# Kernel tuning notes

Hardware: AMD Instinct MI355X
Metric: run time of the kernel (lower is better)

Reference implementation:

```python
import jax
import jax.numpy as jnp
from jax import lax
import numpy as np

B, C, Hsp, Wsp = 16, 256, 64, 64
E, HID = 4, 128          # num_experts, expert_hidden
RH = 128                 # router_hidden
TOP_K = 1
EPS = 1e-9


def setup_inputs() -> dict:
    key = jax.random.key(0)
    ks = jax.random.split(key, 8)
    s = lambda *shape: 1.0 / np.sqrt(shape[-1])
    x = jax.random.normal(ks[0], (B, C, Hsp, Wsp), dtype=jnp.float32)
    # router: Linear(C->RH), Linear(RH->E)
    Wr1 = jax.random.normal(ks[1], (RH, C), dtype=jnp.float32) * s(RH, C)
    br1 = jnp.zeros((RH,), dtype=jnp.float32)
    Wr2 = jax.random.normal(ks[2], (E, RH), dtype=jnp.float32) * s(E, RH)
    br2 = jnp.zeros((E,), dtype=jnp.float32)
    # experts (stacked over E): 1x1 C->HID, 3x3 HID->HID, 1x1 HID->C, all bias-free
    W1 = jax.random.normal(ks[3], (E, HID, C), dtype=jnp.float32) * s(E, HID, C)
    W2 = jax.random.normal(ks[4], (E, HID, HID, 3, 3), dtype=jnp.float32) * (1.0 / np.sqrt(HID * 9))
    W3 = jax.random.normal(ks[5], (E, C, HID), dtype=jnp.float32) * s(E, C, HID)
    return {"x": x, "Wr1": Wr1, "br1": br1, "Wr2": Wr2, "br2": br2,
            "W1": W1, "W2": W2, "W3": W3}


def reference(x, Wr1, br1, Wr2, br2, W1, W2, W3):
    b = x.shape[0]
    # --- router on globally pooled features ---
    pooled = x.mean(axis=(2, 3))                      # [B, C]
    h = jax.nn.relu(pooled @ Wr1.T + br1)             # [B, RH]
    logits = h @ Wr2.T + br2                          # [B, E]
    probs = jax.nn.softmax(logits, axis=1)
    # top-k masking + renormalize (top_k < num_experts)
    vals, idx = lax.top_k(probs, TOP_K)               # [B, k]
    mask = jnp.zeros_like(probs).at[jnp.arange(b)[:, None], idx].set(vals)
    probs = mask / (mask.sum(axis=1, keepdims=True) + EPS)
    # --- run all experts (as in original) ---
    # 1x1 conv C->HID, per expert:  [B, E, HID, H, W]
    y1 = jax.nn.relu(jnp.einsum('bcij,ehc->behij', x, W1))
    # 3x3 grouped conv (one group per expert), HID->HID
    y1m = y1.reshape(b, E * HID, Hsp, Wsp)
    y2 = lax.conv_general_dilated(
        y1m, W2.reshape(E * HID, HID, 3, 3),
        window_strides=(1, 1), padding='SAME',
        feature_group_count=E,
        dimension_numbers=('NCHW', 'OIHW', 'NCHW'))
    y2 = jax.nn.relu(y2).reshape(b, E, HID, Hsp, Wsp)
    # 1x1 conv HID->C fused with routed weighted sum over experts + residual
    out = jnp.einsum('begij,ecg,be->bcij', y2, W3, probs) + x
    return out
```

## Files before the change

kernel.cpp:

```cpp
#include <hip/hip_runtime.h>

typedef unsigned short ushort_t;
typedef unsigned int uint32;
typedef __attribute__((ext_vector_type(8))) short s16x8;
typedef __attribute__((ext_vector_type(4))) float f32x4;

#define BB   16
#define CC   256
#define NPX  4096
#define EE   4
#define HID  128
#define RHH  128
#define PW   66
#define PPX  (66*66)

__device__ __forceinline__ ushort_t f2bf(float f) {
  uint32 x = __float_as_uint(f);
  x += 0x7fffu + ((x >> 16) & 1u);
  return (ushort_t)(x >> 16);
}
__device__ __forceinline__ void g2l16(const void* g, void* l) {
  __builtin_amdgcn_global_load_lds((const __attribute__((address_space(1))) uint32*)g,
                                   (__attribute__((address_space(3))) uint32*)l, 16, 0, 0);
}

__global__ __launch_bounds__(256)
void k_prep(const float* __restrict__ x, float* __restrict__ pooled,
            const float* __restrict__ W1f, const float* __restrict__ W3f,
            const float* __restrict__ W2f, ushort_t* __restrict__ W1b,
            ushort_t* __restrict__ W3b, ushort_t* __restrict__ W2r,
            ushort_t* __restrict__ y1Tp) {
  int bid = blockIdx.x, t = threadIdx.x;
  if (bid < 4096) {
    int c = bid & 255, b = bid >> 8;
    const float* xg = x + ((size_t)b * CC + c) * NPX;
    float s = 0.f;
#pragma unroll
    for (int k = 0; k < 4; ++k) {
      float4 v = *(const float4*)(xg + (size_t)(k * 256 + t) * 4);
      s += v.x + v.y + v.z + v.w;
    }
#pragma unroll
    for (int o = 32; o >= 1; o >>= 1) s += __shfl_down(s, o, 64);
    __shared__ float wsum[4];
    if ((t & 63) == 0) wsum[t >> 6] = s;
    __syncthreads();
    if (t == 0) pooled[(size_t)b * CC + c] = wsum[0] + wsum[1] + wsum[2] + wsum[3];
  } else if (bid < 4352) {
    int i4 = ((bid - 4096) * 256 + t) * 4;
    const float* src; ushort_t* dst; int off;
    if (i4 < EE * HID * CC) { src = W1f; dst = W1b; off = i4; }
    else { src = W3f; dst = W3b; off = i4 - EE * HID * CC; }
    float4 v = *(const float4*)(src + off);
    ushort4 o;
    o.x = f2bf(v.x); o.y = f2bf(v.y); o.z = f2bf(v.z); o.w = f2bf(v.w);
    *(ushort4*)(dst + off) = o;
  } else if (bid < 6656) {
    int i = (bid - 4352) * 256 + t;
    int h = i & 127;
    int g = (i >> 7) & 127;
    int et = i >> 14;
    int tap = et % 9;
    int e = et / 9;
    W2r[i] = f2bf(W2f[((((size_t)e * 128 + g) * 128 + h) * 3 + tap / 3) * 3 + tap % 3]);
  } else {
    int p = (bid - 6656) * 8 + (t >> 5);
    int b = p / 260, i = p % 260;
    int row, col;
    if (i < 66)       { row = 0;       col = i; }
    else if (i < 132) { row = 65;      col = i - 66; }
    else if (i < 196) { row = i - 131; col = 0; }
    else              { row = i - 195; col = 65; }
    uint2* dst = (uint2*)(y1Tp + (((size_t)b * PPX + row * PW + col) * HID) + (t & 31) * 4);
    *dst = make_uint2(0u, 0u);
  }
}

__global__ __launch_bounds__(128)
void k_router(const float* __restrict__ pooled, const float* __restrict__ Wr1,
              const float* __restrict__ br1, const float* __restrict__ Wr2,
              const float* __restrict__ br2, int* __restrict__ eidx,
              float* __restrict__ gatew) {
  int b = blockIdx.x, t = threadIdx.x;
  __shared__ float spool[CC];
  __shared__ float hb[RHH];
  __shared__ float lg[EE];
  for (int cc = t; cc < CC; cc += 128) spool[cc] = pooled[(size_t)b * CC + cc];
  __syncthreads();
  float s0 = 0.f;
  const float* wr = Wr1 + t * CC;
  for (int c = 0; c < CC; ++c) s0 += spool[c] * wr[c];
  float a = br1[t] + s0 * (1.0f / NPX);
  hb[t] = a > 0.f ? a : 0.f;
  __syncthreads();
  if (t < EE) {
    float s = br2[t];
    const float* w2 = Wr2 + t * RHH;
    for (int r = 0; r < RHH; ++r) s += hb[r] * w2[r];
    lg[t] = s;
  }
  __syncthreads();
  if (t == 0) {
    float m = lg[0]; int mi = 0;
    for (int e = 1; e < EE; ++e) if (lg[e] > m) { m = lg[e]; mi = e; }
    float den = 0.f;
    for (int e = 0; e < EE; ++e) den += expf(lg[e] - m);
    float v = 1.0f / den;
    eidx[b] = mi;
    gatew[b] = v / (v + 1e-9f);
  }
}

#define STAGE64(dstA, srcA_expr, dstB, srcB_expr)                         \
  {                                                                       \
    _Pragma("unroll")                                                     \
    for (int s_ = 0; s_ < 4; ++s_) {                                      \
      int ch_ = wave * 4 + s_;                                            \
      int r = ch_ * 8 + (lane >> 3);                                      \
      int kc = ((lane & 7) ^ (lane >> 3)) * 8;                            \
      g2l16(srcA_expr, &dstA[ch_ * 512]);                                 \
      g2l16(srcB_expr, &dstB[ch_ * 512]);                                 \
    }                                                                     \
  }

#define STAGE64B(dstB, srcB_expr)                                         \
  {                                                                       \
    _Pragma("unroll")                                                     \
    for (int s_ = 0; s_ < 4; ++s_) {                                      \
      int ch_ = wave * 4 + s_;                                            \
      int r = ch_ * 8 + (lane >> 3);                                      \
      int kc = ((lane & 7) ^ (lane >> 3)) * 8;                            \
      g2l16(srcB_expr, &dstB[ch_ * 512]);                                 \
    }                                                                     \
  }

#define MFMA64(At_, Bt_, ACC_)                                            \
  _Pragma("unroll")                                                       \
  for (int kh = 0; kh < 2; ++kh) {                                        \
    s16x8 af[4], bfr[4];                                                  \
    int cidx = ((kh * 4 + (lane >> 4)) ^ (lane & 7)) * 8;                 \
    _Pragma("unroll")                                                     \
    for (int i = 0; i < 4; ++i)                                           \
      af[i] = *(const s16x8*)&At_[(wm + i * 16 + (lane & 15)) * 64 + cidx]; \
    _Pragma("unroll")                                                     \
    for (int j = 0; j < 4; ++j)                                           \
      bfr[j] = *(const s16x8*)&Bt_[(wn + j * 16 + (lane & 15)) * 64 + cidx]; \
    _Pragma("unroll")                                                     \
    for (int i = 0; i < 4; ++i)                                           \
      _Pragma("unroll")                                                   \
      for (int j = 0; j < 4; ++j)                                         \
        ACC_[i][j] = __builtin_amdgcn_mfma_f32_16x16x32_bf16(af[i], bfr[j], ACC_[i][j], 0, 0, 0); \
  }

__global__ __launch_bounds__(256)
void k_conv1(const float* __restrict__ x, const ushort_t* __restrict__ W1b,
             const int* __restrict__ eidx, ushort_t* __restrict__ y1Tp) {
  int mt = blockIdx.x, b = blockIdx.y;
  int e = eidx[b];
  int t = threadIdx.x, wave = t >> 6, lane = t & 63;
  int wm = (wave & 1) * 64, wn = (wave >> 1) * 64;
  __shared__ ushort_t smem[128 * 128];
  ushort_t* At = smem;
  ushort_t* Bt = smem + 128 * 64;
  f32x4 acc[4][4] = {};
  const float* xg = x + (size_t)b * CC * NPX + mt * 128;
  const ushort_t* w1 = W1b + (size_t)e * HID * CC;

  int cp = t >> 3;
  int kk = cp * 2;
  int pxb = (t & 7) * 4;

  for (int ks = 0; ks < 4; ++ks) {
    int k0 = ks * 64;
    __syncthreads();
    STAGE64B(Bt, w1 + (size_t)r * CC + k0 + kc);
    {
      const float* r0 = xg + (size_t)(k0 + kk) * NPX;
      const float* r1 = r0 + NPX;
#pragma unroll
      for (int i = 0; i < 4; ++i) {
        int p = pxb + i * 32;
        float4 va = *(const float4*)(r0 + p);
        float4 vb = *(const float4*)(r1 + p);
#pragma unroll
        for (int q = 0; q < 4; ++q) {
          int m = p + q;
          uint32 v = (uint32)f2bf(((const float*)&va)[q]) |
                     ((uint32)f2bf(((const float*)&vb)[q]) << 16);
          int us = m * 64 + (((kk >> 3) ^ (m & 7)) << 3) + (kk & 7);
          *(uint32*)&At[us] = v;
        }
      }
    }
    __syncthreads();
    MFMA64(At, Bt, acc);
  }
  __syncthreads();
#pragma unroll
  for (int i = 0; i < 4; ++i)
#pragma unroll
    for (int j = 0; j < 4; ++j)
#pragma unroll
      for (int r = 0; r < 4; ++r) {
        int m = wm + i * 16 + (lane >> 4) * 4 + r;
        int n = wn + j * 16 + (lane & 15);
        float v = acc[i][j][r];
        smem[m * 128 + (((n >> 3) ^ (m & 7)) << 3) + (n & 7)] = f2bf(v > 0.f ? v : 0.f);
      }
  __syncthreads();
  ushort_t* yb = y1Tp + (size_t)b * PPX * HID;
#pragma unroll
  for (int it = 0; it < 8; ++it) {
    int idx = it * 256 + t;
    int row = idx >> 4, ch = idx & 15;
    int prow = mt * 2 + (row >> 6) + 1, pcol = (row & 63) + 1;
    uint4 v = *(const uint4*)&smem[row * 128 + ((ch ^ (row & 7)) << 3)];
    *(uint4*)(yb + ((size_t)prow * PW + pcol) * HID + ch * 8) = v;
  }
}

__global__ __launch_bounds__(256, 2)
void k_conv23(const ushort_t* __restrict__ y1Tp, const ushort_t* __restrict__ W2r,
              const ushort_t* __restrict__ W3b, const float* __restrict__ x,
              const int* __restrict__ eidx, const float* __restrict__ gatew,
              float* __restrict__ out) {
  int mt = blockIdx.x, b = blockIdx.y;
  int e = eidx[b];
  float gw = gatew[b];
  int t = threadIdx.x, wave = t >> 6, lane = t & 63;
  int wm = (wave & 1) * 64, wn = (wave >> 1) * 64;
  __shared__ ushort_t bufA[128 * 64];
  __shared__ ushort_t bufB[128 * 64];
  __shared__ ushort_t y2s[2][128 * 64];
  const ushort_t* yb = y1Tp + (size_t)b * PPX * HID;
  const ushort_t* w2e = W2r + (size_t)e * 9 * HID * HID;

  f32x4 acc[4][4] = {};
  for (int tap = 0; tap < 9; ++tap) {
    int dy = tap / 3 - 1, dx = tap % 3 - 1;
    const ushort_t* w2t = w2e + tap * HID * HID;
#pragma unroll
    for (int ks = 0; ks < 2; ++ks) {
      int k0 = ks * 64;
      __syncthreads();
      STAGE64(bufA, yb + ((size_t)(mt * 2 + (r >> 6) + 1 + dy) * PW + (r & 63) + 1 + dx) * HID + k0 + kc,
              bufB, w2t + (size_t)r * HID + k0 + kc);
      __syncthreads();
      MFMA64(bufA, bufB, acc);
    }
  }
#pragma unroll
  for (int i = 0; i < 4; ++i)
#pragma unroll
    for (int j = 0; j < 4; ++j)
#pragma unroll
      for (int r = 0; r < 4; ++r) {
        int m = wm + i * 16 + (lane >> 4) * 4 + r;
        int n = wn + j * 16 + (lane & 15);
        float v = acc[i][j][r];
        ushort_t bv = f2bf(v > 0.f ? v : 0.f);
        int nn = n & 63;
        ushort_t* buf = (n < 64) ? y2s[0] : y2s[1];
        buf[m * 64 + ((nn >> 3) ^ (m & 7)) * 8 + (nn & 7)] = bv;
      }
  __syncthreads();
  f32x4 acc3[2][4][4] = {};
  const ushort_t* w3 = W3b + (size_t)e * CC * HID;
#pragma unroll
  for (int h = 0; h < 2; ++h) {
#pragma unroll
    for (int ks = 0; ks < 2; ++ks) {
      ushort_t* bt = (ks == 0) ? bufA : bufB;
      STAGE64B(bt, w3 + (size_t)(h * 128 + r) * HID + ks * 64 + kc);
      __syncthreads();
      MFMA64(y2s[ks], bt, acc3[h]);
    }
  }
  float* Tf = (float*)y2s;
  for (int h = 0; h < 2; ++h) {
    for (int jj = 0; jj < 4; ++jj) {
      __syncthreads();
      if ((wn >> 6) == (jj >> 1)) {
        int j0 = (jj & 1) * 2;
#pragma unroll
        for (int jd = 0; jd < 2; ++jd) {
          int cl = jd * 16 + (lane & 15);
#pragma unroll
          for (int i = 0; i < 4; ++i) {
            int pb = wm + i * 16 + (lane >> 4) * 4;
            *(f32x4*)&Tf[cl * 132 + pb] = acc3[h][i][j0 + jd];
          }
        }
      }
      __syncthreads();
#pragma unroll
      for (int it = 0; it < 4; ++it) {
        int idx = it * 256 + t;
        int crow = idx >> 5;
        int p4 = (idx & 31) * 4;
        int c = h * 128 + jj * 32 + crow;
        int px = mt * 128 + p4;
        size_t base = ((size_t)b * CC + c) * NPX + px;
        f32x4 vv = *(const f32x4*)&Tf[crow * 132 + p4];
        f32x4 xa = *(const f32x4*)(x + base);
        vv = gw * vv + xa;
        __builtin_nontemporal_store(vv, (f32x4*)(out + base));
      }
    }
  }
}

extern "C" void kernel_launch(void* const* d_in, const int* in_sizes, int n_in,
                              void* d_out, int out_size, void* d_ws, size_t ws_size,
                              hipStream_t stream) {
  const float* x   = (const float*)d_in[0];
  const float* Wr1 = (const float*)d_in[1];
  const float* br1 = (const float*)d_in[2];
  const float* Wr2 = (const float*)d_in[3];
  const float* br2 = (const float*)d_in[4];
  const float* W1  = (const float*)d_in[5];
  const float* W2  = (const float*)d_in[6];
  const float* W3  = (const float*)d_in[7];
  float* out = (float*)d_out;

  char* ws = (char*)d_ws;
  int*      eidx   = (int*)ws;
  float*    gatew  = (float*)(ws + 64);
  float*    pooled = (float*)(ws + 256);
  ushort_t* W1b    = (ushort_t*)(ws + 16640);
  ushort_t* W3b    = (ushort_t*)(ws + 278784);
  ushort_t* W2r    = (ushort_t*)(ws + 540928);
  ushort_t* y1Tp   = (ushort_t*)(ws + 1720576);

  k_prep  <<<7176, 256, 0, stream>>>(x, pooled, W1, W3, W2, W1b, W3b, W2r, y1Tp);
  k_router<<<16, 128, 0, stream>>>(pooled, Wr1, br1, Wr2, br2, eidx, gatew);
  k_conv1 <<<dim3(32, 16), 256, 0, stream>>>(x, W1b, eidx, y1Tp);
  k_conv23<<<dim3(32, 16), 256, 0, stream>>>(y1Tp, W2r, W3b, x, eidx, gatew, out);
}
```

Baseline: 186.7 us.

## Stage halo tile once per K-half and double-buffer 3x3 weights in conv23

The 3x3 conv now loads a 4-row by 66-column halo of y1 into LDS once per 64-channel half and reads all nine shifted taps from it, instead of re-staging the activation tile for every tap. Weight tiles for successive taps are double-buffered, with the next load issued before the current MFMAs and guarded by explicit vmcnt waits and raw barriers. The W2 repack in the prep kernel is also rewritten so each thread reads contiguous 9-tap groups for two input channels and writes packed pairs, which cuts that section's block count. The changes reduce global/L2 traffic and barrier count, but the manual waitcnt/barrier scheduling and the swizzled halo indexing are fragile.

```diff
diff --git a/kernel.cpp b/kernel.cpp
--- a/kernel.cpp
+++ b/kernel.cpp
@@ -55,16 +55,22 @@
     ushort4 o;
     o.x = f2bf(v.x); o.y = f2bf(v.y); o.z = f2bf(v.z); o.w = f2bf(v.w);
     *(ushort4*)(dst + off) = o;
-  } else if (bid < 6656) {
-    int i = (bid - 4352) * 256 + t;
-    int h = i & 127;
-    int g = (i >> 7) & 127;
-    int et = i >> 14;
-    int tap = et % 9;
-    int e = et / 9;
-    W2r[i] = f2bf(W2f[((((size_t)e * 128 + g) * 128 + h) * 3 + tap / 3) * 3 + tap % 3]);
+  } else if (bid < 4480) {
+    int idx = (bid - 4352) * 256 + t;
+    int e = idx >> 13;
+    int o = (idx >> 6) & 127;
+    int ip = (idx & 63) * 2;
+    const float* s0 = W2f + ((size_t)((e * 128 + o) * 128) + ip) * 9;
+    float v0[9], v1[9];
+#pragma unroll
+    for (int tp = 0; tp < 9; ++tp) { v0[tp] = s0[tp]; v1[tp] = s0[9 + tp]; }
+#pragma unroll
+    for (int tp = 0; tp < 9; ++tp) {
+      uint32 w = (uint32)f2bf(v0[tp]) | ((uint32)f2bf(v1[tp]) << 16);
+      *(uint32*)&W2r[(((size_t)(e * 9 + tp) * 128 + o) * 128) + ip] = w;
+    }
   } else {
-    int p = (bid - 6656) * 8 + (t >> 5);
+    int p = (bid - 4480) * 8 + (t >> 5);
     int b = p / 260, i = p % 260;
     int row, col;
     if (i < 66)       { row = 0;       col = i; }
@@ -111,18 +117,6 @@
   }
 }
 
-#define STAGE64(dstA, srcA_expr, dstB, srcB_expr)                         \
-  {                                                                       \
-    _Pragma("unroll")                                                     \
-    for (int s_ = 0; s_ < 4; ++s_) {                                      \
-      int ch_ = wave * 4 + s_;                                            \
-      int r = ch_ * 8 + (lane >> 3);                                      \
-      int kc = ((lane & 7) ^ (lane >> 3)) * 8;                            \
-      g2l16(srcA_expr, &dstA[ch_ * 512]);                                 \
-      g2l16(srcB_expr, &dstB[ch_ * 512]);                                 \
-    }                                                                     \
-  }
-
 #define STAGE64B(dstB, srcB_expr)                                         \
   {                                                                       \
     _Pragma("unroll")                                                     \
@@ -134,6 +128,17 @@
     }                                                                     \
   }
 
+#define STAGEW(dst, wsrc, k0v)                                            \
+  {                                                                       \
+    _Pragma("unroll")                                                     \
+    for (int s_ = 0; s_ < 4; ++s_) {                                      \
+      int ch_ = wave * 4 + s_;                                            \
+      int r_ = ch_ * 8 + (lane >> 3);                                     \
+      int kc_ = ((lane & 7) ^ (lane >> 3)) * 8;                           \
+      g2l16(wsrc + (size_t)r_ * HID + (k0v) + kc_, &dst[ch_ * 512]);      \
+    }                                                                     \
+  }
+
 #define MFMA64(At_, Bt_, ACC_)                                            \
   _Pragma("unroll")                                                       \
   for (int kh = 0; kh < 2; ++kh) {                                        \
@@ -150,6 +155,29 @@
       _Pragma("unroll")                                                   \
       for (int j = 0; j < 4; ++j)                                         \
         ACC_[i][j] = __builtin_amdgcn_mfma_f32_16x16x32_bf16(af[i], bfr[j], ACC_[i][j], 0, 0, 0); \
+  }
+
+#define MFMA64H(Hs_, dyv, dxv, Bt_, ACC_)                                 \
+  {                                                                       \
+    int hbase = ((wm >> 6) + 1 + (dyv)) * 66 + (lane & 15) + 1 + (dxv);   \
+    _Pragma("unroll")                                                     \
+    for (int kh = 0; kh < 2; ++kh) {                                      \
+      s16x8 af[4], bfr[4];                                                \
+      int clog = kh * 4 + (lane >> 4);                                    \
+      int aoff = (clog ^ (hbase & 7)) << 3;                               \
+      int cidx = (clog ^ (lane & 7)) << 3;                                \
+      _Pragma("unroll")                                                   \
+      for (int i = 0; i < 4; ++i)                                         \
+        af[i] = *(const s16x8*)&Hs_[(hbase + i * 16) * 64 + aoff];        \
+      _Pragma("unroll")                                                   \
+      for (int j = 0; j < 4; ++j)                                         \
+        bfr[j] = *(const s16x8*)&Bt_[(wn + j * 16 + (lane & 15)) * 64 + cidx]; \
+      _Pragma("unroll")                                                   \
+      for (int i = 0; i < 4; ++i)                                         \
+        _Pragma("unroll")                                                 \
+        for (int j = 0; j < 4; ++j)                                       \
+          ACC_[i][j] = __builtin_amdgcn_mfma_f32_16x16x32_bf16(af[i], bfr[j], ACC_[i][j], 0, 0, 0); \
+    }                                                                     \
   }
 
 __global__ __launch_bounds__(256)
@@ -229,26 +257,44 @@
   float gw = gatew[b];
   int t = threadIdx.x, wave = t >> 6, lane = t & 63;
   int wm = (wave & 1) * 64, wn = (wave >> 1) * 64;
-  __shared__ ushort_t bufA[128 * 64];
-  __shared__ ushort_t bufB[128 * 64];
-  __shared__ ushort_t y2s[2][128 * 64];
+  __shared__ ushort_t Hs[4 * 66 * 64];
+  __shared__ ushort_t Wb0[128 * 64];
+  __shared__ ushort_t Wb1[128 * 64];
   const ushort_t* yb = y1Tp + (size_t)b * PPX * HID;
   const ushort_t* w2e = W2r + (size_t)e * 9 * HID * HID;
+  asm volatile("" :: "v"(gw), "s"(e));
 
   f32x4 acc[4][4] = {};
-  for (int tap = 0; tap < 9; ++tap) {
-    int dy = tap / 3 - 1, dx = tap % 3 - 1;
-    const ushort_t* w2t = w2e + tap * HID * HID;
-#pragma unroll
-    for (int ks = 0; ks < 2; ++ks) {
-      int k0 = ks * 64;
-      __syncthreads();
-      STAGE64(bufA, yb + ((size_t)(mt * 2 + (r >> 6) + 1 + dy) * PW + (r & 63) + 1 + dx) * HID + k0 + kc,
-              bufB, w2t + (size_t)r * HID + k0 + kc);
-      __syncthreads();
-      MFMA64(bufA, bufB, acc);
-    }
-  }
+  for (int ks = 0; ks < 2; ++ks) {
+    int k0 = ks * 64;
+    __syncthreads();
+#pragma unroll
+    for (int it = 0; it < 9; ++it) {
+      if (it < 8 || wave == 0) {
+        int q = it * 256 + t;
+        int p = q >> 3, slot = q & 7;
+        g2l16(yb + ((size_t)(mt * 132 + p)) * HID + k0 + ((slot ^ (p & 7)) << 3),
+              &Hs[(it * 256 + wave * 64) * 8]);
+      }
+    }
+    STAGEW(Wb0, w2e + 0 * HID * HID, k0);
+    __syncthreads();
+#pragma unroll
+    for (int tap = 0; tap < 9; ++tap) {
+      ushort_t* cur = (tap & 1) ? Wb1 : Wb0;
+      ushort_t* nxt = (tap & 1) ? Wb0 : Wb1;
+      if (tap < 8) {
+        STAGEW(nxt, w2e + (tap + 1) * HID * HID, k0);
+        asm volatile("s_waitcnt vmcnt(4)" ::: "memory");
+      } else {
+        asm volatile("s_waitcnt vmcnt(0)" ::: "memory");
+      }
+      __builtin_amdgcn_s_barrier();
+      MFMA64H(Hs, tap / 3 - 1, tap % 3 - 1, cur, acc);
+      __builtin_amdgcn_s_barrier();
+    }
+  }
+  ushort_t (*y2s)[128 * 64] = (ushort_t (*)[128 * 64])Hs;
 #pragma unroll
   for (int i = 0; i < 4; ++i)
 #pragma unroll
@@ -263,20 +309,19 @@
         ushort_t* buf = (n < 64) ? y2s[0] : y2s[1];
         buf[m * 64 + ((nn >> 3) ^ (m & 7)) * 8 + (nn & 7)] = bv;
       }
-  __syncthreads();
   f32x4 acc3[2][4][4] = {};
   const ushort_t* w3 = W3b + (size_t)e * CC * HID;
 #pragma unroll
   for (int h = 0; h < 2; ++h) {
 #pragma unroll
     for (int ks = 0; ks < 2; ++ks) {
-      ushort_t* bt = (ks == 0) ? bufA : bufB;
-      STAGE64B(bt, w3 + (size_t)(h * 128 + r) * HID + ks * 64 + kc);
+      ushort_t* bt = (ks == 0) ? Wb0 : Wb1;
+      STAGEW(bt, w3 + (size_t)h * 128 * HID, ks * 64);
       __syncthreads();
       MFMA64(y2s[ks], bt, acc3[h]);
     }
   }
-  float* Tf = (float*)y2s;
+  float* Tf = (float*)Hs;
   for (int h = 0; h < 2; ++h) {
     for (int jj = 0; jj < 4; ++jj) {
       __syncthreads();
@@ -332,7 +377,7 @@
   ushort_t* W2r    = (ushort_t*)(ws + 540928);
   ushort_t* y1Tp   = (ushort_t*)(ws + 1720576);
 
-  k_prep  <<<7176, 256, 0, stream>>>(x, pooled, W1, W3, W2, W1b, W3b, W2r, y1Tp);
+  k_prep  <<<5000, 256, 0, stream>>>(x, pooled, W1, W3, W2, W1b, W3b, W2r, y1Tp);
   k_router<<<16, 128, 0, stream>>>(pooled, Wr1, br1, Wr2, br2, eidx, gatew);
   k_conv1 <<<dim3(32, 16), 256, 0, stream>>>(x, W1b, eidx, y1Tp);
   k_conv23<<<dim3(32, 16), 256, 0, stream>>>(y1Tp, W2r, W3b, x, eidx, gatew, out);
```

Result: no change. 184.7 us (-1.0%).
